# Kernel optimization log

Hardware: AMD Instinct MI355X
Metric: run time of the kernel (lower is better)

The kernel has to match this reference:

```python
import jax, jax.numpy as jnp
import numpy as np

MULT = 32       # multiplicity per irrep type (both input and output)
N = 262144      # number of nodes/examples
LS = (0, 1, 2, 3)  # irrep degrees -> block sizes 2l+1 = 1,3,5,7


def setup_inputs() -> dict:
    key = jax.random.key(0)
    keys = jax.random.split(key, 2 * len(LS))
    inp = {}
    for j, l in enumerate(LS):
        m = 2 * l + 1
        inp[f"x{l}"] = jax.random.normal(keys[2 * j], (N, MULT, m), dtype=jnp.float32)
        inp[f"W{l}"] = jax.random.normal(keys[2 * j + 1], (MULT, MULT, m), dtype=jnp.float32)
    return inp


def reference(x0, x1, x2, x3, W0, W1, W2, W3):
    # Block-diagonal equivariant linear: for each irrep type l,
    # out[n, o, m] = sum_i W_l[o, i, m] * x_l[n, i, m]
    # (elementwise in m within each 2l+1 block, summed over input multiplicity i).
    outs = [
        jnp.einsum("nim,oim->nom", x, W)
        for x, W in ((x0, W0), (x1, W1), (x2, W2), (x3, W3))
    ]
    # Concatenate flattened irrep blocks -> [N, MULT*(1+3+5+7)] = [N, 512]
    return jnp.concatenate([o.reshape(o.shape[0], -1) for o in outs], axis=-1)
```

## Files before the change

kernel.cpp:

```cpp
#include <hip/hip_runtime.h>
#include <hip/hip_fp16.h>


#define NTH 512
#define TN  32

typedef _Float16 f16x8 __attribute__((ext_vector_type(8)));
typedef float    f32x4 __attribute__((ext_vector_type(4)));

#define LGKM0_BAR() do { asm volatile("s_waitcnt lgkmcnt(0)" ::: "memory"); \
                         __builtin_amdgcn_s_barrier(); } while (0)

template<int M_, int PB>
__device__ __forceinline__ void stageW(const float* __restrict__ src,
                                       __half* __restrict__ dst, int tid)
{
    #pragma unroll
    for (int it = 0; it < (256 * M_ + NTH - 1) / NTH; ++it) {
        const int f = tid + it * NTH;
        if (f < 256 * M_) {
            float4 v = ((const float4*)src)[f];
            const float vf[4] = {v.x, v.y, v.z, v.w};
            const int e0 = 4 * f;
            #pragma unroll
            for (int k = 0; k < 4; ++k) {
                const int e = e0 + k;
                const int o = e / (32 * M_);
                const int r = e - o * (32 * M_);
                const int i = r / M_, mi = r - i * M_;
                const int p = PB + mi;
                dst[p * 1280 + o * 40 + ((i + 8 * p) & 31)] = __float2half(vf[k]);
            }
        }
    }
}

template<int M_, int PB>
__device__ __forceinline__ void mkoff(int tloc, int* offk)
{
    const int e0    = 4 * tloc;
    const int nodel = e0 / (32 * M_);
    const int r0    = e0 - nodel * (32 * M_);
    #pragma unroll
    for (int k = 0; k < 4; ++k) {
        const int ii = (r0 + k) / M_, mi = (r0 + k) - ii * M_;
        const int p  = PB + mi;
        offk[k] = p * 1280 + nodel * 40 + ((ii + 8 * p) & 31);
    }
}

__device__ __forceinline__ void plane_info(int p, int& Mm, int& BASE, int& MI)
{
    if (p == 0)     { Mm = 1; BASE = 0;   MI = 0;     }
    else if (p < 4) { Mm = 3; BASE = 32;  MI = p - 1; }
    else if (p < 9) { Mm = 5; BASE = 128; MI = p - 4; }
    else            { Mm = 7; BASE = 288; MI = p - 9; }
}

__device__ __forceinline__ void store_tile(const __half* __restrict__ OC,
                                           float* __restrict__ dst, int tid)
{
    #pragma unroll
    for (int it = 0; it < 4; ++it) {
        const int d0   = 8 * tid + 4096 * it;
        const int node = d0 >> 9, col = d0 & 511;
        uint4 h8 = *(const uint4*)(OC + node * 520 + col);
        const __half2* hp = (const __half2*)&h8;
        float2 f0 = __half22float2(hp[0]);
        float2 f1 = __half22float2(hp[1]);
        float2 f2 = __half22float2(hp[2]);
        float2 f3 = __half22float2(hp[3]);
        *(float4*)(dst + d0)     = make_float4(f0.x, f0.y, f1.x, f1.y);
        *(float4*)(dst + d0 + 4) = make_float4(f2.x, f2.y, f3.x, f3.y);
    }
}

__global__ __launch_bounds__(NTH, 4) void eqlin(
    const float* __restrict__ x0, const float* __restrict__ x1,
    const float* __restrict__ x2, const float* __restrict__ x3,
    const float* __restrict__ w0, const float* __restrict__ w1,
    const float* __restrict__ w2, const float* __restrict__ w3,
    float* __restrict__ out, int n_tiles)
{
    __shared__ __align__(16) __half XT[20480];
    __shared__ __align__(16) __half OC[16640];
    const int tid  = threadIdx.x;
    const int wave = tid >> 6;
    const int lane = tid & 63;

    int thrg, Mg, offk[4];
    const float* xb;
    bool isM1 = false;
    if (tid < 32)       { thrg = 32;  Mg = 1; xb = x0; mkoff<1, 0>(tid,       offk); isM1 = true; }
    else if (tid < 128) { thrg = 96;  Mg = 3; xb = x1; mkoff<3, 1>(tid - 32,  offk); }
    else if (tid < 288) { thrg = 160; Mg = 5; xb = x2; mkoff<5, 4>(tid - 128, offk); }
    else                { thrg = 224; Mg = 7; xb = x3; mkoff<7, 9>(tid - 288, offk); }
    const int  tloc    = (tid < 32) ? tid : (tid < 128) ? tid - 32 : (tid < 288) ? tid - 128 : tid - 288;
    const long jstride = 4L * thrg;
    const long tstride = (long)gridDim.x * 1024L * Mg;

    const float* srcp = xb + (long)blockIdx.x * (1024L * Mg) + 4 * tloc;
    float4 pf[8];
    #pragma unroll
    for (int j = 0; j < 8; ++j)
        pf[j] = *(const float4*)(srcp + j * jstride);

    stageW<1, 0>(w0, XT, tid);
    stageW<3, 1>(w1, XT, tid);
    stageW<5, 4>(w2, XT, tid);
    stageW<7, 9>(w3, XT, tid);

    const int lrow = lane & 15;
    const int lk8  = (lane >> 4) * 8;
    const int crow = (lane >> 4) * 4;
    const int p0   = wave * 2, p1 = wave * 2 + 1;
    const int c0   = (lk8 + 8 * p0) & 31;
    const int c1   = (lk8 + 8 * p1) & 31;

    LGKM0_BAR();
    f16x8 Wf[2][2];
    Wf[0][0] = *(const f16x8*)(XT + p0 * 1280 + lrow * 40 + c0);
    Wf[0][1] = *(const f16x8*)(XT + p0 * 1280 + (lrow + 16) * 40 + c0);
    Wf[1][0] = *(const f16x8*)(XT + p1 * 1280 + lrow * 40 + c1);
    Wf[1][1] = *(const f16x8*)(XT + p1 * 1280 + (lrow + 16) * 40 + c1);
    LGKM0_BAR();

    int Mm0, BASE0, MI0, Mm1, BASE1, MI1;
    plane_info(p0, Mm0, BASE0, MI0);
    plane_info(p1, Mm1, BASE1, MI1);

    long prev_node0 = -1;
    for (int t = blockIdx.x; t < n_tiles; t += gridDim.x) {
        const long node0 = (long)t * TN;

        if (prev_node0 >= 0)
            store_tile(OC, out + prev_node0 * 512, tid);

        #pragma unroll
        for (int j = 0; j < 8; ++j) {
            const float4 v = pf[j];
            const int jb = j * 160;
            if (isM1) {
                __half2* p = (__half2*)&XT[offk[0] + jb];
                p[0] = __floats2half2_rn(v.x, v.y);
                p[1] = __floats2half2_rn(v.z, v.w);
            } else {
                XT[offk[0] + jb] = __float2half(v.x);
                XT[offk[1] + jb] = __float2half(v.y);
                XT[offk[2] + jb] = __float2half(v.z);
                XT[offk[3] + jb] = __float2half(v.w);
            }
        }
        if (t + (long)gridDim.x < n_tiles) {
            srcp += tstride;
            #pragma unroll
            for (int j = 0; j < 8; ++j)
                pf[j] = *(const float4*)(srcp + j * jstride);
        }

        LGKM0_BAR();

        f32x4 acc[2][2][2] = {};
        {
            const __half* xp0 = XT + p0 * 1280 + lrow * 40 + c0;
            const __half* xp1 = XT + p1 * 1280 + lrow * 40 + c1;
            f16x8 A00 = *(const f16x8*)xp0;
            f16x8 A01 = *(const f16x8*)(xp0 + 640);
            f16x8 A10 = *(const f16x8*)xp1;
            f16x8 A11 = *(const f16x8*)(xp1 + 640);
            acc[0][0][0] = __builtin_amdgcn_mfma_f32_16x16x32_f16(A00, Wf[0][0], acc[0][0][0], 0, 0, 0);
            acc[0][0][1] = __builtin_amdgcn_mfma_f32_16x16x32_f16(A00, Wf[0][1], acc[0][0][1], 0, 0, 0);
            acc[0][1][0] = __builtin_amdgcn_mfma_f32_16x16x32_f16(A01, Wf[0][0], acc[0][1][0], 0, 0, 0);
            acc[0][1][1] = __builtin_amdgcn_mfma_f32_16x16x32_f16(A01, Wf[0][1], acc[0][1][1], 0, 0, 0);
            acc[1][0][0] = __builtin_amdgcn_mfma_f32_16x16x32_f16(A10, Wf[1][0], acc[1][0][0], 0, 0, 0);
            acc[1][0][1] = __builtin_amdgcn_mfma_f32_16x16x32_f16(A10, Wf[1][1], acc[1][0][1], 0, 0, 0);
            acc[1][1][0] = __builtin_amdgcn_mfma_f32_16x16x32_f16(A11, Wf[1][0], acc[1][1][0], 0, 0, 0);
            acc[1][1][1] = __builtin_amdgcn_mfma_f32_16x16x32_f16(A11, Wf[1][1], acc[1][1][1], 0, 0, 0);
        }
        #pragma unroll
        for (int pl = 0; pl < 2; ++pl) {
            const int Mm   = pl ? Mm1   : Mm0;
            const int BASE = pl ? BASE1 : BASE0;
            const int MI   = pl ? MI1   : MI0;
            #pragma unroll
            for (int nh = 0; nh < 2; ++nh)
            #pragma unroll
            for (int oh = 0; oh < 2; ++oh) {
                const int o     = oh * 16 + lrow;
                const int colb  = BASE + o * Mm + MI;
                const int nodeb = nh * 16 + crow;
                #pragma unroll
                for (int r = 0; r < 4; ++r)
                    OC[(nodeb + r) * 520 + colb] = __float2half(acc[pl][nh][oh][r]);
            }
        }

        LGKM0_BAR();
        prev_node0 = node0;
    }

    if (prev_node0 >= 0)
        store_tile(OC, out + prev_node0 * 512, tid);
}

extern "C" void kernel_launch(void* const* d_in, const int* in_sizes, int n_in,
                              void* d_out, int out_size, void* d_ws, size_t ws_size,
                              hipStream_t stream)
{
    long tot = 0;
    for (int i = 0; i < n_in; ++i) tot += in_sizes[i];
    const long N = (tot - 16384) / 512;
    const int  ms[4] = {1, 3, 5, 7};
    const float* xs[4]  = {nullptr, nullptr, nullptr, nullptr};
    const float* wsp[4] = {nullptr, nullptr, nullptr, nullptr};
    for (int i = 0; i < n_in; ++i) {
        const long s = in_sizes[i];
        for (int l = 0; l < 4; ++l) {
            if (s == N * 32 * ms[l])      xs[l]  = (const float*)d_in[i];
            else if (s == 1024L * ms[l])  wsp[l] = (const float*)d_in[i];
        }
    }
    const int n_tiles = (int)(N / TN);
    const int grid = 1024;
    hipLaunchKernelGGL(eqlin, dim3(grid), dim3(NTH), 0, stream,
                       xs[0], xs[1], xs[2], xs[3],
                       wsp[0], wsp[1], wsp[2], wsp[3],
                       (float*)d_out, n_tiles);
}
```

Before: 218.2 us.

## Halve block to 256 threads and 16-node tiles with four planes per wave

Shrinks the workgroup to 256 threads and the node tile to 16, halving shared memory per block so more blocks can be resident per CU. Each wave now owns four weight planes, which are staged in two halves because the smaller XT buffer cannot hold the full weights at once. The store of the previous tile moves after the next prefetch is issued, to overlap global stores with loads. Each tile carries half the work, so barrier and loop overhead per node doubles, and the grid stays at 1024 blocks, so each block runs twice as many tiles.

```diff
diff --git a/kernel.cpp b/kernel.cpp
--- a/kernel.cpp
+++ b/kernel.cpp
@@ -2,8 +2,8 @@
 #include <hip/hip_fp16.h>
 
 
-#define NTH 512
-#define TN  32
+#define NTH 256
+#define TN  16
 
 typedef _Float16 f16x8 __attribute__((ext_vector_type(8)));
 typedef float    f32x4 __attribute__((ext_vector_type(4)));
@@ -12,13 +12,13 @@
                          __builtin_amdgcn_s_barrier(); } while (0)
 
 template<int M_, int PB>
-__device__ __forceinline__ void stageW(const float* __restrict__ src,
-                                       __half* __restrict__ dst, int tid)
-{
-    #pragma unroll
-    for (int it = 0; it < (256 * M_ + NTH - 1) / NTH; ++it) {
+__device__ __forceinline__ void stageWhalf(const float* __restrict__ src,
+                                           __half* __restrict__ dst, int tid)
+{
+    #pragma unroll
+    for (int it = 0; it < (128 * M_ + NTH - 1) / NTH; ++it) {
         const int f = tid + it * NTH;
-        if (f < 256 * M_) {
+        if (f < 128 * M_) {
             float4 v = ((const float4*)src)[f];
             const float vf[4] = {v.x, v.y, v.z, v.w};
             const int e0 = 4 * f;
@@ -29,7 +29,7 @@
                 const int r = e - o * (32 * M_);
                 const int i = r / M_, mi = r - i * M_;
                 const int p = PB + mi;
-                dst[p * 1280 + o * 40 + ((i + 8 * p) & 31)] = __float2half(vf[k]);
+                dst[p * 640 + o * 40 + ((i + 8 * p) & 31)] = __float2half(vf[k]);
             }
         }
     }
@@ -45,7 +45,7 @@
     for (int k = 0; k < 4; ++k) {
         const int ii = (r0 + k) / M_, mi = (r0 + k) - ii * M_;
         const int p  = PB + mi;
-        offk[k] = p * 1280 + nodel * 40 + ((ii + 8 * p) & 31);
+        offk[k] = p * 640 + nodel * 40 + ((ii + 8 * p) & 31);
     }
 }
 
@@ -62,7 +62,7 @@
 {
     #pragma unroll
     for (int it = 0; it < 4; ++it) {
-        const int d0   = 8 * tid + 4096 * it;
+        const int d0   = 8 * tid + 2048 * it;
         const int node = d0 >> 9, col = d0 & 511;
         uint4 h8 = *(const uint4*)(OC + node * 520 + col);
         const __half2* hp = (const __half2*)&h8;
@@ -82,8 +82,8 @@
     const float* __restrict__ w2, const float* __restrict__ w3,
     float* __restrict__ out, int n_tiles)
 {
-    __shared__ __align__(16) __half XT[20480];
-    __shared__ __align__(16) __half OC[16640];
+    __shared__ __align__(16) __half XT[10240];
+    __shared__ __align__(16) __half OC[8320];
     const int tid  = threadIdx.x;
     const int wave = tid >> 6;
     const int lane = tid & 63;
@@ -91,55 +91,54 @@
     int thrg, Mg, offk[4];
     const float* xb;
     bool isM1 = false;
-    if (tid < 32)       { thrg = 32;  Mg = 1; xb = x0; mkoff<1, 0>(tid,       offk); isM1 = true; }
-    else if (tid < 128) { thrg = 96;  Mg = 3; xb = x1; mkoff<3, 1>(tid - 32,  offk); }
-    else if (tid < 288) { thrg = 160; Mg = 5; xb = x2; mkoff<5, 4>(tid - 128, offk); }
-    else                { thrg = 224; Mg = 7; xb = x3; mkoff<7, 9>(tid - 288, offk); }
-    const int  tloc    = (tid < 32) ? tid : (tid < 128) ? tid - 32 : (tid < 288) ? tid - 128 : tid - 288;
+    if (tid < 16)       { thrg = 16;  Mg = 1; xb = x0; mkoff<1, 0>(tid,       offk); isM1 = true; }
+    else if (tid < 64)  { thrg = 48;  Mg = 3; xb = x1; mkoff<3, 1>(tid - 16,  offk); }
+    else if (tid < 144) { thrg = 80;  Mg = 5; xb = x2; mkoff<5, 4>(tid - 64,  offk); }
+    else                { thrg = 112; Mg = 7; xb = x3; mkoff<7, 9>(tid - 144, offk); }
+    const int  tloc    = (tid < 16) ? tid : (tid < 64) ? tid - 16 : (tid < 144) ? tid - 64 : tid - 144;
     const long jstride = 4L * thrg;
-    const long tstride = (long)gridDim.x * 1024L * Mg;
-
-    const float* srcp = xb + (long)blockIdx.x * (1024L * Mg) + 4 * tloc;
+    const long tstride = (long)gridDim.x * 512L * Mg;
+
+    const float* srcp = xb + (long)blockIdx.x * (512L * Mg) + 4 * tloc;
     float4 pf[8];
     #pragma unroll
     for (int j = 0; j < 8; ++j)
         pf[j] = *(const float4*)(srcp + j * jstride);
-
-    stageW<1, 0>(w0, XT, tid);
-    stageW<3, 1>(w1, XT, tid);
-    stageW<5, 4>(w2, XT, tid);
-    stageW<7, 9>(w3, XT, tid);
 
     const int lrow = lane & 15;
     const int lk8  = (lane >> 4) * 8;
     const int crow = (lane >> 4) * 4;
-    const int p0   = wave * 2, p1 = wave * 2 + 1;
-    const int c0   = (lk8 + 8 * p0) & 31;
-    const int c1   = (lk8 + 8 * p1) & 31;
-
-    LGKM0_BAR();
-    f16x8 Wf[2][2];
-    Wf[0][0] = *(const f16x8*)(XT + p0 * 1280 + lrow * 40 + c0);
-    Wf[0][1] = *(const f16x8*)(XT + p0 * 1280 + (lrow + 16) * 40 + c0);
-    Wf[1][0] = *(const f16x8*)(XT + p1 * 1280 + lrow * 40 + c1);
-    Wf[1][1] = *(const f16x8*)(XT + p1 * 1280 + (lrow + 16) * 40 + c1);
-    LGKM0_BAR();
-
-    int Mm0, BASE0, MI0, Mm1, BASE1, MI1;
-    plane_info(p0, Mm0, BASE0, MI0);
-    plane_info(p1, Mm1, BASE1, MI1);
+    const int pA = wave * 4, pB = pA + 1, pC = pA + 2, pD = pA + 3;
+    const int cs[4] = { (lk8 + 8 * pA) & 31, (lk8 + 8 * pB) & 31,
+                        (lk8 + 8 * pC) & 31, (lk8 + 8 * pD) & 31 };
+
+    f16x8 Wf[4][2];
+    #pragma unroll
+    for (int half = 0; half < 2; ++half) {
+        const int o0 = half * 16;
+        stageWhalf<1, 0>(w0 + (long)o0 * 32,  XT, tid);
+        stageWhalf<3, 1>(w1 + (long)o0 * 96,  XT, tid);
+        stageWhalf<5, 4>(w2 + (long)o0 * 160, XT, tid);
+        stageWhalf<7, 9>(w3 + (long)o0 * 224, XT, tid);
+        LGKM0_BAR();
+        #pragma unroll
+        for (int pl = 0; pl < 4; ++pl)
+            Wf[pl][half] = *(const f16x8*)(XT + (pA + pl) * 640 + lrow * 40 + cs[pl]);
+        LGKM0_BAR();
+    }
+
+    int Mm[4], BASE[4], MI[4];
+    #pragma unroll
+    for (int pl = 0; pl < 4; ++pl) plane_info(pA + pl, Mm[pl], BASE[pl], MI[pl]);
 
     long prev_node0 = -1;
     for (int t = blockIdx.x; t < n_tiles; t += gridDim.x) {
         const long node0 = (long)t * TN;
 
-        if (prev_node0 >= 0)
-            store_tile(OC, out + prev_node0 * 512, tid);
-
         #pragma unroll
         for (int j = 0; j < 8; ++j) {
             const float4 v = pf[j];
-            const int jb = j * 160;
+            const int jb = j * 80;
             if (isM1) {
                 __half2* p = (__half2*)&XT[offk[0] + jb];
                 p[0] = __floats2half2_rn(v.x, v.y);
@@ -157,42 +156,27 @@
             for (int j = 0; j < 8; ++j)
                 pf[j] = *(const float4*)(srcp + j * jstride);
         }
-
-        LGKM0_BAR();
-
-        f32x4 acc[2][2][2] = {};
-        {
-            const __half* xp0 = XT + p0 * 1280 + lrow * 40 + c0;
-            const __half* xp1 = XT + p1 * 1280 + lrow * 40 + c1;
-            f16x8 A00 = *(const f16x8*)xp0;
-            f16x8 A01 = *(const f16x8*)(xp0 + 640);
-            f16x8 A10 = *(const f16x8*)xp1;
-            f16x8 A11 = *(const f16x8*)(xp1 + 640);
-            acc[0][0][0] = __builtin_amdgcn_mfma_f32_16x16x32_f16(A00, Wf[0][0], acc[0][0][0], 0, 0, 0);
-            acc[0][0][1] = __builtin_amdgcn_mfma_f32_16x16x32_f16(A00, Wf[0][1], acc[0][0][1], 0, 0, 0);
-            acc[0][1][0] = __builtin_amdgcn_mfma_f32_16x16x32_f16(A01, Wf[0][0], acc[0][1][0], 0, 0, 0);
-            acc[0][1][1] = __builtin_amdgcn_mfma_f32_16x16x32_f16(A01, Wf[0][1], acc[0][1][1], 0, 0, 0);
-            acc[1][0][0] = __builtin_amdgcn_mfma_f32_16x16x32_f16(A10, Wf[1][0], acc[1][0][0], 0, 0, 0);
-            acc[1][0][1] = __builtin_amdgcn_mfma_f32_16x16x32_f16(A10, Wf[1][1], acc[1][0][1], 0, 0, 0);
-            acc[1][1][0] = __builtin_amdgcn_mfma_f32_16x16x32_f16(A11, Wf[1][0], acc[1][1][0], 0, 0, 0);
-            acc[1][1][1] = __builtin_amdgcn_mfma_f32_16x16x32_f16(A11, Wf[1][1], acc[1][1][1], 0, 0, 0);
-        }
-        #pragma unroll
-        for (int pl = 0; pl < 2; ++pl) {
-            const int Mm   = pl ? Mm1   : Mm0;
-            const int BASE = pl ? BASE1 : BASE0;
-            const int MI   = pl ? MI1   : MI0;
+        if (prev_node0 >= 0)
+            store_tile(OC, out + prev_node0 * 512, tid);
+
+        LGKM0_BAR();
+
+        f32x4 acc[4][2] = {};
+        #pragma unroll
+        for (int pl = 0; pl < 4; ++pl) {
+            f16x8 A = *(const f16x8*)(XT + (pA + pl) * 640 + lrow * 40 + cs[pl]);
+            acc[pl][0] = __builtin_amdgcn_mfma_f32_16x16x32_f16(A, Wf[pl][0], acc[pl][0], 0, 0, 0);
+            acc[pl][1] = __builtin_amdgcn_mfma_f32_16x16x32_f16(A, Wf[pl][1], acc[pl][1], 0, 0, 0);
+        }
+        #pragma unroll
+        for (int pl = 0; pl < 4; ++pl)
+        #pragma unroll
+        for (int oh = 0; oh < 2; ++oh) {
+            const int o    = oh * 16 + lrow;
+            const int colb = BASE[pl] + o * Mm[pl] + MI[pl];
             #pragma unroll
-            for (int nh = 0; nh < 2; ++nh)
-            #pragma unroll
-            for (int oh = 0; oh < 2; ++oh) {
-                const int o     = oh * 16 + lrow;
-                const int colb  = BASE + o * Mm + MI;
-                const int nodeb = nh * 16 + crow;
-                #pragma unroll
-                for (int r = 0; r < 4; ++r)
-                    OC[(nodeb + r) * 520 + colb] = __float2half(acc[pl][nh][oh][r]);
-            }
+            for (int r = 0; r < 4; ++r)
+                OC[(crow + r) * 520 + colb] = __float2half(acc[pl][oh][r]);
         }
 
         LGKM0_BAR();
```

Measured after the change: 224.9 us. +3.1%, slower.
